# Kernel optimization log

Hardware: AMD Instinct MI355X
Metric: run time of the kernel (lower is better)

## Reference

```python
import jax, jax.numpy as jnp
import numpy as np

H = 128          # hidden / embed dim
NH = 4           # attention heads
HD = H // NH     # head dim = 32
MFD = 4          # missile feat dim
FOD = 15         # full obs dim
NEG_SLOPE = 0.01 # LeakyReLU default


def _gru(x_seq, h0, wih, whh, bih, bhh):
    # x_seq: [B,S,H], h0: [B,H]; torch GRU gate math
    def step(h, x):
        gi = x @ wih.T + bih            # [B,3H]
        gh = h @ whh.T + bhh
        i_r, i_z, i_n = jnp.split(gi, 3, axis=-1)
        h_r, h_z, h_n = jnp.split(gh, 3, axis=-1)
        r = jax.nn.sigmoid(i_r + h_r)
        z = jax.nn.sigmoid(i_z + h_z)
        n = jnp.tanh(i_n + r * h_n)
        h_new = (1.0 - z) * n + z * h
        return h_new, h_new
    h_last, outs = jax.lax.scan(step, h0, jnp.swapaxes(x_seq, 0, 1))
    return jnp.swapaxes(outs, 0, 1), h_last  # [B,S,H], [B,H]


def _ln(x, w, b, eps=1e-5):
    mu = jnp.mean(x, axis=-1, keepdims=True)
    var = jnp.var(x, axis=-1, keepdims=True)
    return (x - mu) * jax.lax.rsqrt(var + eps) * w + b


def setup_inputs() -> dict:
    key = jax.random.key(0)
    ks = jax.random.split(key, 24)
    B, S = 4096, 64
    s = 0.02
    p = {
        "obs": jax.random.normal(ks[0], (B, S, FOD), jnp.float32),
        "h0": jnp.zeros((1, B, H), jnp.float32),
        "enc_air_w": jax.random.normal(ks[1], (H, FOD)) * s,
        "enc_air_b": jnp.zeros((H,)),
        "enc_m_w": jax.random.normal(ks[2], (H, MFD)) * s,
        "enc_m_b": jnp.zeros((H,)),
        "gru_wih": jax.random.normal(ks[3], (3 * H, H)) * s,
        "gru_whh": jax.random.normal(ks[4], (3 * H, H)) * s,
        "gru_bih": jnp.zeros((3 * H,)),
        "gru_bhh": jnp.zeros((3 * H,)),
        "qln_w": jnp.ones((H,)), "qln_b": jnp.zeros((H,)),
        "kln_w": jnp.ones((H,)), "kln_b": jnp.zeros((H,)),
        "attn_in_w": jax.random.normal(ks[5], (3 * H, H)) * s,
        "attn_in_b": jnp.zeros((3 * H,)),
        "attn_out_w": jax.random.normal(ks[6], (H, H)) * s,
        "attn_out_b": jnp.zeros((H,)),
        "mlp0_w": jax.random.normal(ks[7], (H, H)) * s,
        "mlp0_b": jnp.zeros((H,)),
        "mlp1_w": jax.random.normal(ks[8], (H, H)) * s,
        "mlp1_b": jnp.zeros((H,)),
        "fco_w": jax.random.normal(ks[9], (1, H)) * s,
        "fco_b": jnp.zeros((1,)),
    }
    return {k: v.astype(jnp.float32) for k, v in p.items()}


def reference(obs, h0, enc_air_w, enc_air_b, enc_m_w, enc_m_b,
              gru_wih, gru_whh, gru_bih, gru_bhh,
              qln_w, qln_b, kln_w, kln_b,
              attn_in_w, attn_in_b, attn_out_w, attn_out_b,
              mlp0_w, mlp0_b, mlp1_w, mlp1_b, fco_w, fco_b):
    B, S, _ = obs.shape
    N = B * S
    # aircraft encoder + GRU with residual
    air_embed = obs @ enc_air_w.T + enc_air_b                      # [B,S,H]
    gru_out, h_last = _gru(air_embed, h0[0], gru_wih, gru_whh, gru_bih, gru_bhh)
    air_feat = (gru_out + air_embed).reshape(N, H)                 # [N,H]
    # missile encoders (shared weights, two missiles)
    m_raw = obs[..., :2 * MFD].reshape(N, 2, MFD)                  # [N,2,4]
    keys_raw = m_raw @ enc_m_w.T + enc_m_b                         # [N,2,H]
    # inactive-missile mask
    inactive = jnp.array([1.0, 0.0, 1.0, 0.0], obs.dtype)
    mask = jnp.all(jnp.isclose(m_raw, inactive, rtol=1e-5, atol=1e-8), axis=-1)  # [N,2]
    # layer norms
    q_n = _ln(air_feat[:, None, :], qln_w, qln_b)                  # [N,1,H]
    k_n = _ln(keys_raw, kln_w, kln_b)                              # [N,2,H]
    # multihead attention (1 query, 2 keys), values are raw keys
    wq, wk, wv = jnp.split(attn_in_w, 3, axis=0)
    bq, bk, bv = jnp.split(attn_in_b, 3, axis=0)
    q = (q_n @ wq.T + bq).reshape(N, 1, NH, HD)
    k = (k_n @ wk.T + bk).reshape(N, 2, NH, HD)
    v = (keys_raw @ wv.T + bv).reshape(N, 2, NH, HD)
    scores = jnp.einsum('nqhd,nkhd->nhqk', q, k) / jnp.sqrt(jnp.float32(HD))
    scores = scores + jnp.where(mask, -jnp.inf, 0.0)[:, None, None, :]
    attn = jax.nn.softmax(scores, axis=-1)                         # [N,NH,1,2]
    ctx = jnp.einsum('nhqk,nkhd->nqhd', attn, v).reshape(N, H)
    attn_out = ctx @ attn_out_w.T + attn_out_b                     # [N,H]
    attn_out = jnp.where(jnp.isnan(attn_out), 0.0, attn_out)       # nan_to_num guard
    combined = air_feat + attn_out
    # MLP head
    h1 = jax.nn.leaky_relu(combined @ mlp0_w.T + mlp0_b, NEG_SLOPE)
    h2 = jax.nn.leaky_relu(h1 @ mlp1_w.T + mlp1_b, NEG_SLOPE)
    val = h2 @ fco_w.T + fco_b                                     # [N,1]
    return val, h_last[None]
```

## Files before the change

### kernel.cpp

```cpp
#include <hip/hip_runtime.h>
#include <math.h>

#define B_   4096
#define S_   64
#define H_   128
#define N_   (B_*S_)

#define WS_WC    0
#define WS_BC    6144
#define WS_WAP   6528
#define WS_WQP   8576
#define WS_SQ    24960
#define WS_EQ    25088
#define WS_KC    25216
#define WS_EK1   25728
#define WS_SK    25856
#define WS_EK2   25984
#define WS_VC    26112
#define WS_VB    26624
#define WS_MV    26752
#define WS_QQ    26756
#define WS_QLIN  26772
#define WS_MBC   26776
#define WS_C0    26777
#define WS_PB    27392
#define WS_WO2T  (WS_PB + 4096)
#define WS_SROW  (WS_PB + 6784)
#define WS_EROW  (WS_PB + 6812)
#define WS_GB    60160
#define WS_AIR   92928
#define TOKS     32

typedef __attribute__((ext_vector_type(8))) short bf16x8;
typedef __attribute__((ext_vector_type(4))) float f32x4;

__device__ __forceinline__ float dot4(float4 a, float4 b){
    return fmaf(a.x,b.x, fmaf(a.y,b.y, fmaf(a.z,b.z, a.w*b.w)));
}
__device__ __forceinline__ unsigned short f2bf(float f){
    union { float f; unsigned u; } v; v.f = f;
    unsigned r = v.u + 0x7FFF + ((v.u >> 16) & 1);
    return (unsigned short)(r >> 16);
}
__device__ __forceinline__ float bf2f(unsigned short u){
    union { unsigned u; float f; } v; v.u = ((unsigned)u) << 16;
    return v.f;
}

__global__ void precompute_kernel(
    const float* __restrict__ enc_air_w, const float* __restrict__ enc_air_b,
    const float* __restrict__ enc_m_w,  const float* __restrict__ enc_m_b,
    const float* __restrict__ gru_wih,  const float* __restrict__ gru_bih,
    const float* __restrict__ qln_w, const float* __restrict__ qln_b,
    const float* __restrict__ kln_w, const float* __restrict__ kln_b,
    const float* __restrict__ attn_in_w, const float* __restrict__ attn_in_b,
    const float* __restrict__ attn_out_w,
    const float* __restrict__ mlp0_w, const float* __restrict__ mlp1_w,
    float* __restrict__ ws)
{
    int i = blockIdx.x*blockDim.x + threadIdx.x;
    if (i < 6144) {
        int o = i>>4, f = i&15; float a = 0.f;
        if (f < 15) for (int k=0;k<128;k++) a = fmaf(gru_wih[o*128+k], enc_air_w[k*15+f], a);
        ws[WS_WC+i] = a;
    } else if (i < 6528) {
        int o = i-6144; float a = gru_bih[o];
        for (int k=0;k<128;k++) a = fmaf(gru_wih[o*128+k], enc_air_b[k], a);
        ws[WS_BC+o] = a;
    } else if (i < 8576) {
        int idx = i-6528; int j = idx>>4, f = idx&15;
        ws[WS_WAP+idx] = (f<15) ? enc_air_w[j*15+f] : 0.f;
    } else if (i < 24960) {
        int idx = i-8576; int o = idx>>7, j = idx&127;
        ws[WS_WQP+idx] = attn_in_w[o*128+j]*qln_w[j];
    } else if (i < 25088) {
        int o = i-24960; float a=0.f;
        for (int j=0;j<128;j++) a = fmaf(attn_in_w[o*128+j], qln_w[j], a);
        ws[WS_SQ+o]=a;
    } else if (i < 25216) {
        int o = i-25088; float a = attn_in_b[o];
        for (int j=0;j<128;j++) a = fmaf(attn_in_w[o*128+j], qln_b[j], a);
        ws[WS_EQ+o]=a;
    } else if (i < 25728) {
        int idx = i-25216; int o = idx>>2, f = idx&3; float a=0.f;
        for (int j=0;j<128;j++) a = fmaf(attn_in_w[(128+o)*128+j]*kln_w[j], enc_m_w[j*4+f], a);
        ws[WS_KC+idx]=a;
    } else if (i < 25856) {
        int o = i-25728; float a=0.f;
        for (int j=0;j<128;j++) a = fmaf(attn_in_w[(128+o)*128+j]*kln_w[j], enc_m_b[j], a);
        ws[WS_EK1+o]=a;
    } else if (i < 25984) {
        int o = i-25856; float a=0.f;
        for (int j=0;j<128;j++) a = fmaf(attn_in_w[(128+o)*128+j], kln_w[j], a);
        ws[WS_SK+o]=a;
    } else if (i < 26112) {
        int o = i-25984; float a = attn_in_b[128+o];
        for (int j=0;j<128;j++) a = fmaf(attn_in_w[(128+o)*128+j], kln_b[j], a);
        ws[WS_EK2+o]=a;
    } else if (i < 26624) {
        int idx = i-26112; int o = idx>>2, f = idx&3; float a=0.f;
        for (int j=0;j<128;j++) a = fmaf(attn_in_w[(256+o)*128+j], enc_m_w[j*4+f], a);
        ws[WS_VC+idx]=a;
    } else if (i < 26752) {
        int o = i-26624; float a = attn_in_b[256+o];
        for (int j=0;j<128;j++) a = fmaf(attn_in_w[(256+o)*128+j], enc_m_b[j], a);
        ws[WS_VB+o]=a;
    } else if (i < 26756) {
        int f = i-26752; float a=0.f;
        for (int j=0;j<128;j++) a += enc_m_w[j*4+f];
        ws[WS_MV+f]=a*(1.f/128.f);
    } else if (i < 26772) {
        int idx = i-26756; int a4 = idx>>2, b4 = idx&3; float a=0.f;
        for (int j=0;j<128;j++) a = fmaf(enc_m_w[j*4+a4], enc_m_w[j*4+b4], a);
        ws[WS_QQ+idx]=a*(1.f/128.f);
    } else if (i < 26776) {
        int f = i-26772; float a=0.f;
        for (int j=0;j<128;j++) a = fmaf(enc_m_b[j], enc_m_w[j*4+f], a);
        ws[WS_QLIN+f]=a*(2.f/128.f);
    } else if (i == 26776) {
        float a=0.f; for (int j=0;j<128;j++) a += enc_m_b[j];
        ws[WS_MBC]=a*(1.f/128.f);
    } else if (i == 26777) {
        float a=0.f; for (int j=0;j<128;j++) a = fmaf(enc_m_b[j], enc_m_b[j], a);
        ws[WS_C0]=a*(1.f/128.f);
    } else if (i >= 32768 && i < 98304) {
        int idx = i - 32768;
        int mm = idx>>14;
        if (mm >= 2) {
            int i8 = idx & 7, l = (idx>>3)&63, p = (idx>>9)&3, wv = (idx>>11)&7;
            int n = 16*wv + (l&15);
            int k = 32*p + ((l>>4)<<3) + i8;
            float v = (mm==2) ? mlp0_w[n*128+k] : mlp1_w[n*128+k];
            ((unsigned short*)(ws+WS_PB))[idx] = f2bf(v);
        }
    }
}

__global__ void pack_gru_kernel(const float* __restrict__ whh, float* __restrict__ ws)
{
    int idx = blockIdx.x*blockDim.x + threadIdx.x;
    int i8 = idx&7, l=(idx>>3)&63, w=(idx>>9)&7, f=idx>>12;
    int n = 16*w + (l&15);
    int k = ((l>>4)<<3) + i8;
    float v = 0.f;
    if (f < 5) {
        int kk = f*32 + k;
        if (kk < 128) v = whh[n*128 + kk];
        else { int kl = kk-128; if (kl<16) v = ws[WS_WC + n*16 + kl]; }
    } else if (f < 10) {
        int kk = (f-5)*32 + k;
        if (kk < 128) v = whh[(128+n)*128 + kk];
        else { int kl = kk-128; if (kl<16) v = ws[WS_WC + (128+n)*16 + kl]; }
    } else if (f < 14) {
        int kk = (f-10)*32 + k;
        v = whh[(256+n)*128 + kk];
    } else if (f == 14) {
        if (k < 16) v = ws[WS_WC + (256+n)*16 + k];
    } else {
        if (k < 16) v = ws[WS_WAP + n*16 + k];
    }
    ((unsigned short*)(ws+WS_GB))[idx] = f2bf(v);
}

__global__ void pack2_kernel(const float* __restrict__ wo, const float* __restrict__ bo,
                             float* __restrict__ ws)
{
    int i = blockIdx.x*blockDim.x + threadIdx.x;
    if (i < 4096) {
        int i8=i&7, l=(i>>3)&63, p=(i>>9)&3, ct=(i>>11)&1;
        int r = 16*ct + (l&15);
        int k = 32*p + ((l>>4)<<3) + i8;
        float v = 0.f;
        if (r < 28){
            int h = r/7, u = r - h*7;
            float a = 0.f;
            for (int d5=0; d5<32; d5++){
                int d = h*32 + d5;
                float c = (u<4) ? ws[WS_KC + d*4 + u]
                        : (u==4) ? ws[WS_EK1 + d]
                        : (u==5) ? ws[WS_SK + d]
                        :          ws[WS_EK2 + d];
                a = fmaf(c, ws[WS_WQP + d*128 + k], a);
            }
            v = a;
        }
        ((unsigned short*)(ws+WS_PB))[i] = f2bf(v);
    } else if (i < 4152) {
        int j = i - 4096; int r = j % 28; int era = j / 28;
        int h = r/7, u = r - h*7;
        float a = 0.f;
        for (int d5=0; d5<32; d5++){
            int d = h*32 + d5;
            float c = (u<4) ? ws[WS_KC + d*4 + u]
                    : (u==4) ? ws[WS_EK1 + d]
                    : (u==5) ? ws[WS_SK + d]
                    :          ws[WS_EK2 + d];
            a = fmaf(c, ws[(era ? WS_EQ : WS_SQ) + d], a);
        }
        ws[(era ? WS_EROW : WS_SROW) + r] = a;
    } else if (i >= 4224 && i < 6912) {
        int j = i - 4224; int c = j>>7, o = j&127;
        float a;
        if (c == 20) a = bo[o];
        else {
            int h = c/5, u = c - h*5;
            a = 0.f;
            for (int d5=0; d5<32; d5++){
                int d = h*32 + d5;
                float cv = (u<4) ? ws[WS_VC + d*4 + u] : ws[WS_VB + d];
                a = fmaf(wo[o*128 + d], cv, a);
            }
        }
        ws[WS_WO2T + c*128 + o] = a;
    }
}

__global__ void pack3_kernel(const float* __restrict__ mlp0_w, float* __restrict__ ws)
{
    int i = blockIdx.x*blockDim.x + threadIdx.x;
    int i8=i&7, l=(i>>3)&63, w=(i>>9)&7;
    int n = 16*w + (l&15);
    int c = ((l>>4)<<3) + i8;
    float v = 0.f;
    if (c < 21){
        float a = 0.f;
        const float* wo2 = ws + WS_WO2T + c*128;
        for (int o=0;o<128;o++) a = fmaf(mlp0_w[n*128+o], wo2[o], a);
        v = a;
    }
    ((unsigned short*)(ws+WS_PB))[4096 + i] = f2bf(v);
}

__global__ __launch_bounds__(512) void gru_kernel(
    const float* __restrict__ obs, const float* __restrict__ h0,
    const float* __restrict__ bhh, const float* __restrict__ ba,
    const float* __restrict__ ws,
    unsigned short* __restrict__ air, float* __restrict__ out)
{
    __shared__ __align__(16) unsigned short Abf[2][16*136];
    __shared__ __align__(16) unsigned short obs_lds[64*16*24];
    __shared__ __align__(16) unsigned short zero16[8];

    const int t = threadIdx.x;
    const int w = t>>6;
    const int l = t&63;
    const int quad = l>>4;
    const int col  = l&15;
    const int jj   = 16*w + col;
    const int row0 = blockIdx.x*16;

    const unsigned short* gb = (const unsigned short*)(ws + WS_GB);
    bf16x8 bf[16];
    #pragma unroll
    for (int f=0; f<16; f++) bf[f] = *(const bf16x8*)&gb[(f*8 + w)*512 + l*8];

    const float bcrt = ws[WS_BC+jj]     + bhh[jj];
    const float bczt = ws[WS_BC+128+jj] + bhh[128+jj];
    const float bcn  = ws[WS_BC+256+jj];
    const float bhn  = bhh[256+jj];
    const float baj  = ba[jj];

    float hreg[4];
    #pragma unroll
    for (int reg=0; reg<4; reg++)
        hreg[reg] = h0[(size_t)(row0+quad*4+reg)*128 + jj];

    if (t < 8) zero16[t] = 0;

    {
        int rr = t>>5, c0 = (t&31)*4;
        float4 hv = *(const float4*)&h0[(size_t)(row0+rr)*128 + c0];
        unsigned long long pk = (unsigned long long)f2bf(hv.x)
              | ((unsigned long long)f2bf(hv.y)<<16)
              | ((unsigned long long)f2bf(hv.z)<<32)
              | ((unsigned long long)f2bf(hv.w)<<48);
        *(unsigned long long*)&Abf[0][rr*136 + c0] = pk;
    }

    #pragma unroll
    for (int it=0; it<8; it++){
        int pair = it*128 + (t>>2);
        int sub  = t&3;
        int tok = pair>>6, s = pair&63;
        const float* op = &obs[((size_t)(row0+tok)*64 + s)*15 + sub*4];
        unsigned long long pk = 0;
        #pragma unroll
        for (int k=0;k<4;k++){
            int c = sub*4+k;
            float ov = (c<15) ? op[k] : 0.f;
            pk |= ((unsigned long long)f2bf(ov)) << (16*k);
        }
        *(unsigned long long*)&obs_lds[(s*16+tok)*24 + sub*4] = pk;
    }
    __syncthreads();

    for (int s=0; s<64; s++){
        const unsigned short* Ac = Abf[s&1];
        unsigned short*       An = Abf[(s+1)&1];

        bf16x8 a0 = *(const bf16x8*)&Ac[col*136 +  0 + quad*8];
        bf16x8 a1 = *(const bf16x8*)&Ac[col*136 + 32 + quad*8];
        bf16x8 a2 = *(const bf16x8*)&Ac[col*136 + 64 + quad*8];
        bf16x8 a3 = *(const bf16x8*)&Ac[col*136 + 96 + quad*8];
        const unsigned short* osrc = (quad<2)
            ? &obs_lds[(s*16+col)*24 + quad*8] : &zero16[0];
        bf16x8 a4 = *(const bf16x8*)osrc;

        f32x4 aR = {0.f,0.f,0.f,0.f};
        f32x4 aZ = {0.f,0.f,0.f,0.f};
        f32x4 aN = {0.f,0.f,0.f,0.f};
        f32x4 aG = {0.f,0.f,0.f,0.f};
        f32x4 aE = {0.f,0.f,0.f,0.f};
        aR = __builtin_amdgcn_mfma_f32_16x16x32_bf16(a0, bf[0],  aR, 0,0,0);
        aR = __builtin_amdgcn_mfma_f32_16x16x32_bf16(a1, bf[1],  aR, 0,0,0);
        aR = __builtin_amdgcn_mfma_f32_16x16x32_bf16(a2, bf[2],  aR, 0,0,0);
        aR = __builtin_amdgcn_mfma_f32_16x16x32_bf16(a3, bf[3],  aR, 0,0,0);
        aR = __builtin_amdgcn_mfma_f32_16x16x32_bf16(a4, bf[4],  aR, 0,0,0);
        aZ = __builtin_amdgcn_mfma_f32_16x16x32_bf16(a0, bf[5],  aZ, 0,0,0);
        aZ = __builtin_amdgcn_mfma_f32_16x16x32_bf16(a1, bf[6],  aZ, 0,0,0);
        aZ = __builtin_amdgcn_mfma_f32_16x16x32_bf16(a2, bf[7],  aZ, 0,0,0);
        aZ = __builtin_amdgcn_mfma_f32_16x16x32_bf16(a3, bf[8],  aZ, 0,0,0);
        aZ = __builtin_amdgcn_mfma_f32_16x16x32_bf16(a4, bf[9],  aZ, 0,0,0);
        aN = __builtin_amdgcn_mfma_f32_16x16x32_bf16(a0, bf[10], aN, 0,0,0);
        aN = __builtin_amdgcn_mfma_f32_16x16x32_bf16(a1, bf[11], aN, 0,0,0);
        aN = __builtin_amdgcn_mfma_f32_16x16x32_bf16(a2, bf[12], aN, 0,0,0);
        aN = __builtin_amdgcn_mfma_f32_16x16x32_bf16(a3, bf[13], aN, 0,0,0);
        aG = __builtin_amdgcn_mfma_f32_16x16x32_bf16(a4, bf[14], aG, 0,0,0);
        aE = __builtin_amdgcn_mfma_f32_16x16x32_bf16(a4, bf[15], aE, 0,0,0);

        #pragma unroll
        for (int reg=0; reg<4; reg++){
            int tok = quad*4 + reg;
            float rg = __builtin_amdgcn_rcpf(1.f + __expf(-(aR[reg] + bcrt)));
            float zg = __builtin_amdgcn_rcpf(1.f + __expf(-(aZ[reg] + bczt)));
            float nx = fmaf(rg, aN[reg] + bhn, aG[reg] + bcn);
            float e2 = __expf(2.f*nx);
            float ng = 1.f - 2.f*__builtin_amdgcn_rcpf(e2 + 1.f);
            float hn = fmaf(zg, hreg[reg]-ng, ng);
            hreg[reg] = hn;
            An[tok*136 + jj] = f2bf(hn);
            air[((size_t)(row0+tok)*64 + s)*128 + jj] = f2bf(hn + (aE[reg] + baj));
        }
        if (s==63){
            #pragma unroll
            for (int reg=0; reg<4; reg++)
                out[(size_t)N_ + (size_t)(row0+quad*4+reg)*128 + jj] = hreg[reg];
        }
        asm volatile("s_waitcnt lgkmcnt(0)" ::: "memory");
        __builtin_amdgcn_s_barrier();
        __builtin_amdgcn_sched_barrier(0);
    }
}

__global__ __launch_bounds__(512) void attnmlp_kernel(
    const float* __restrict__ obs,
    const float* __restrict__ ws,
    const float* __restrict__ b0, const float* __restrict__ b1,
    const float* __restrict__ fcw, const float* __restrict__ fcb,
    const unsigned short* __restrict__ air, float* __restrict__ out)
{
    __shared__ __align__(16) unsigned short U_bf[TOKS*168];
    __shared__ __align__(16) unsigned short H1_bf[TOKS*136];
    __shared__ float praw[TOKS*28];
    __shared__ float obs_m[TOKS][8];
    __shared__ float mu_s[TOKS], rs_s[TOKS];
    __shared__ float kmu_s[TOKS][2], krs_s[TOKS][2];
    __shared__ int   kmask_s[TOKS][2];

    const int t = threadIdx.x;
    const int w = t>>6;
    const int l = t&63;
    const int quad = l>>4;
    const int col  = l&15;
    const int jj   = 16*w + col;
    const int n0 = blockIdx.x*TOKS;

    const unsigned short* pb = (const unsigned short*)(ws + WS_PB);

    {
        const int tok0 = t>>4, sub = t&15;
        const unsigned short* ap = &air[(size_t)(n0+tok0)*128 + sub*8];
        uint4 xv = *(const uint4*)ap;
        *(uint4*)&U_bf[tok0*168 + sub*8] = xv;
        float sm = 0.f, s2 = 0.f;
        #pragma unroll
        for (int q4=0;q4<4;q4++){
            unsigned qv = ((const unsigned*)&xv)[q4];
            float a = bf2f((unsigned short)(qv & 0xFFFF));
            float b = bf2f((unsigned short)(qv >> 16));
            sm += a + b;
            s2 = fmaf(a,a, fmaf(b,b, s2));
        }
        #pragma unroll
        for (int m=1;m<16;m<<=1){ sm += __shfl_xor(sm,m); s2 += __shfl_xor(s2,m); }
        if (sub==0){
            float mu = sm*(1.f/128.f);
            float var = s2*(1.f/128.f) - mu*mu;
            mu_s[tok0]=mu; rs_s[tok0]=rsqrtf(var+1e-5f);
        }
        if (sub<5){
            #pragma unroll
            for (int c=0;c<4;c++) U_bf[tok0*168 + 148 + sub*4 + c] = 0;
        }
        if (sub<8) obs_m[tok0][sub] = obs[(size_t)(n0+tok0)*15 + sub];
    }
    if (t < 64){
        int rr = t>>1, mi = t&1;
        const float* mp = &obs[(size_t)(n0+rr)*15 + mi*4];
        float m0=mp[0], m1=mp[1], m2=mp[2], m3=mp[3];
        const float tol1 = 1e-8f + 1e-5f, tol0 = 1e-8f;
        kmask_s[rr][mi] = (fabsf(m0-1.f)<=tol1)&&(fabsf(m1)<=tol0)&&
                          (fabsf(m2-1.f)<=tol1)&&(fabsf(m3)<=tol0);
        float mv[4]={m0,m1,m2,m3};
        float mu = ws[WS_MBC];
        #pragma unroll
        for (int f=0;f<4;f++) mu = fmaf(ws[WS_MV+f], mv[f], mu);
        float e2 = ws[WS_C0];
        #pragma unroll
        for (int a4=0;a4<4;a4++){
            e2 = fmaf(ws[WS_QLIN+a4], mv[a4], e2);
            #pragma unroll
            for (int b4=0;b4<4;b4++) e2 = fmaf(ws[WS_QQ+a4*4+b4]*mv[a4], mv[b4], e2);
        }
        float var = e2 - mu*mu;
        kmu_s[rr][mi]=mu; krs_s[rr][mi]=rsqrtf(var+1e-5f);
    }
    __syncthreads();

    if (w < 4){
        const int tt = w>>1, ct = w&1;
        const int jA = ct*16 + col;
        f32x4 acc = {0.f,0.f,0.f,0.f};
        #pragma unroll
        for (int p=0;p<4;p++){
            bf16x8 a = *(const bf16x8*)&U_bf[(tt*16+col)*168 + p*32 + quad*8];
            bf16x8 b = *(const bf16x8*)&pb[((ct*4+p)*64 + l)*8];
            acc = __builtin_amdgcn_mfma_f32_16x16x32_bf16(a, b, acc, 0,0,0);
        }
        if (jA < 28){
            const float Sr = ws[WS_SROW + jA], Er = ws[WS_EROW + jA];
            #pragma unroll
            for (int reg=0;reg<4;reg++){
                int tok = tt*16 + quad*4 + reg;
                praw[tok*28 + jA] = fmaf(rs_s[tok], acc[reg] - mu_s[tok]*Sr, Er);
            }
        }
    }
    __syncthreads();

    if (t < TOKS*4){
        const int tok = t>>2, h = t&3;
        const float* pr = &praw[tok*28 + h*7];
        const float T0=pr[0],T1=pr[1],T2=pr[2],T3=pr[3],Pa=pr[4],Pb=pr[5],Pc=pr[6];
        const float4 m0v = *(const float4*)&obs_m[tok][0];
        const float4 m1v = *(const float4*)&obs_m[tok][4];
        const float scale = 0.17677669529663687f;
        float d0 = fmaf(T0,m0v.x, fmaf(T1,m0v.y, fmaf(T2,m0v.z, fmaf(T3,m0v.w, Pa))));
        float d1 = fmaf(T0,m1v.x, fmaf(T1,m1v.y, fmaf(T2,m1v.z, fmaf(T3,m1v.w, Pa))));
        float s0 = fmaf(krs_s[tok][0], d0 - kmu_s[tok][0]*Pb, Pc) * scale;
        float s1 = fmaf(krs_s[tok][1], d1 - kmu_s[tok][1]*Pb, Pc) * scale;
        int msk0 = kmask_s[tok][0], msk1 = kmask_s[tok][1];
        float a0, a1;
        if (msk0 && msk1){
            a0=0.f; a1=0.f;
            if (h==0) U_bf[tok*168 + 148] = 0;
        } else {
            if (h==0) U_bf[tok*168 + 148] = 0x3F80;
            if (msk0)      { a0=0.f; a1=1.f; }
            else if (msk1) { a0=1.f; a1=0.f; }
            else {
                float mx = fmaxf(s0,s1);
                float e0 = __expf(s0-mx), e1 = __expf(s1-mx);
                float inv = 1.f/(e0+e1);
                a0 = e0*inv; a1 = e1*inv;
            }
        }
        int cb = tok*168 + 128 + h*5;
        U_bf[cb+0] = f2bf(fmaf(a0, m0v.x, a1*m1v.x));
        U_bf[cb+1] = f2bf(fmaf(a0, m0v.y, a1*m1v.y));
        U_bf[cb+2] = f2bf(fmaf(a0, m0v.z, a1*m1v.z));
        U_bf[cb+3] = f2bf(fmaf(a0, m0v.w, a1*m1v.w));
        U_bf[cb+4] = f2bf(a0 + a1);
    }
    __syncthreads();

    {
        bf16x8 bfr[5];
        #pragma unroll
        for (int p=0;p<4;p++) bfr[p] = *(const bf16x8*)&pb[((2*32 + w*4 + p)*64 + l)*8];
        bfr[4] = *(const bf16x8*)&pb[4096 + (w*64 + l)*8];
        f32x4 acc[2];
        #pragma unroll
        for (int tt=0;tt<2;tt++) acc[tt] = (f32x4){0.f,0.f,0.f,0.f};
        #pragma unroll
        for (int p=0;p<5;p++){
            const int ko = p*32 + quad*8;
            #pragma unroll
            for (int tt=0;tt<2;tt++){
                bf16x8 a = *(const bf16x8*)&U_bf[(tt*16+col)*168 + ko];
                acc[tt] = __builtin_amdgcn_mfma_f32_16x16x32_bf16(a, bfr[p], acc[tt], 0,0,0);
            }
        }
        const float b0j = b0[jj];
        #pragma unroll
        for (int tt=0;tt<2;tt++){
            #pragma unroll
            for (int reg=0;reg<4;reg++){
                int tok = tt*16 + quad*4 + reg;
                float v = acc[tt][reg] + b0j;
                v = (v > 0.f) ? v : 0.01f*v;
                H1_bf[tok*136 + jj] = f2bf(v);
            }
        }
    }
    __syncthreads();

    {
        bf16x8 bfr[4];
        #pragma unroll
        for (int p=0;p<4;p++) bfr[p] = *(const bf16x8*)&pb[((3*32 + w*4 + p)*64 + l)*8];
        f32x4 acc[2];
        #pragma unroll
        for (int tt=0;tt<2;tt++) acc[tt] = (f32x4){0.f,0.f,0.f,0.f};
        #pragma unroll
        for (int p=0;p<4;p++){
            const int ko = p*32 + quad*8;
            #pragma unroll
            for (int tt=0;tt<2;tt++){
                bf16x8 a = *(const bf16x8*)&H1_bf[(tt*16+col)*136 + ko];
                acc[tt] = __builtin_amdgcn_mfma_f32_16x16x32_bf16(a, bfr[p], acc[tt], 0,0,0);
            }
        }
        const float b1j = b1[jj], fcj = fcw[jj];
        float pv[8];
        #pragma unroll
        for (int tt=0;tt<2;tt++){
            #pragma unroll
            for (int reg=0;reg<4;reg++){
                float v = acc[tt][reg] + b1j;
                v = (v > 0.f) ? v : 0.01f*v;
                pv[tt*4+reg] = v * fcj;
            }
        }
        #pragma unroll
        for (int m=1;m<16;m<<=1){
            #pragma unroll
            for (int q2=0;q2<8;q2++) pv[q2] += __shfl_xor(pv[q2], m);
        }
        if (col==0){
            #pragma unroll
            for (int tt=0;tt<2;tt++){
                #pragma unroll
                for (int reg=0;reg<4;reg++)
                    praw[(tt*16 + quad*4 + reg)*8 + w] = pv[tt*4+reg];
            }
        }
    }
    __syncthreads();

    if (t < TOKS){
        float a = fcb[0];
        #pragma unroll
        for (int k=0;k<8;k++) a += praw[t*8 + k];
        out[n0 + t] = a;
    }
}

extern "C" void kernel_launch(void* const* d_in, const int* in_sizes, int n_in,
                              void* d_out, int out_size, void* d_ws, size_t ws_size,
                              hipStream_t stream) {
    const float* obs       = (const float*)d_in[0];
    const float* h0        = (const float*)d_in[1];
    const float* enc_air_w = (const float*)d_in[2];
    const float* enc_air_b = (const float*)d_in[3];
    const float* enc_m_w   = (const float*)d_in[4];
    const float* enc_m_b   = (const float*)d_in[5];
    const float* gru_wih   = (const float*)d_in[6];
    const float* gru_whh   = (const float*)d_in[7];
    const float* gru_bih   = (const float*)d_in[8];
    const float* gru_bhh   = (const float*)d_in[9];
    const float* qln_w     = (const float*)d_in[10];
    const float* qln_b     = (const float*)d_in[11];
    const float* kln_w     = (const float*)d_in[12];
    const float* kln_b     = (const float*)d_in[13];
    const float* attn_in_w = (const float*)d_in[14];
    const float* attn_in_b = (const float*)d_in[15];
    const float* attn_out_w= (const float*)d_in[16];
    const float* attn_out_b= (const float*)d_in[17];
    const float* mlp0_w    = (const float*)d_in[18];
    const float* mlp0_b    = (const float*)d_in[19];
    const float* mlp1_w    = (const float*)d_in[20];
    const float* mlp1_b    = (const float*)d_in[21];
    const float* fco_w     = (const float*)d_in[22];
    const float* fco_b     = (const float*)d_in[23];
    float* out = (float*)d_out;
    float* ws  = (float*)d_ws;
    unsigned short* air = (unsigned short*)(ws + WS_AIR);

    precompute_kernel<<<dim3(384), dim3(256), 0, stream>>>(
        enc_air_w, enc_air_b, enc_m_w, enc_m_b, gru_wih, gru_bih,
        qln_w, qln_b, kln_w, kln_b, attn_in_w, attn_in_b,
        attn_out_w, mlp0_w, mlp1_w, ws);

    pack_gru_kernel<<<dim3(256), dim3(256), 0, stream>>>(gru_whh, ws);
    pack2_kernel<<<dim3(27), dim3(256), 0, stream>>>(attn_out_w, attn_out_b, ws);
    pack3_kernel<<<dim3(16), dim3(256), 0, stream>>>(mlp0_w, ws);

    gru_kernel<<<dim3(256), dim3(512), 0, stream>>>(
        obs, h0, gru_bhh, enc_air_b, ws, air, out);

    attnmlp_kernel<<<dim3(N_/TOKS), dim3(512), 0, stream>>>(
        obs, ws, mlp0_b, mlp1_b, fco_w, fco_b, air, out);
}
```

Measured before the change: 251.4 us.

## Pipeline GRU input MFMAs, double attn-MLP tile, move LN stats and final projection to MFMA

The GRU loop now computes the obs-projection MFMAs for step s+1 during step s, so they leave the recurrent critical path. It also strength-reduces the air store address and writes the final hidden state once after the loop. The attention/MLP kernel processes 64 tokens per block instead of 32. Layer-norm sum and sum-of-squares are computed with MFMAs (a ones column in the packed weights plus a self-product), replacing shuffle reductions. The final fc dot product becomes an MFMA against a packed fco_w matrix instead of a cross-lane shuffle reduction. These cut per-step latency and reduction overhead, at the cost of more registers and LDS per block and a changed workspace layout.

```diff
diff --git a/kernel.cpp b/kernel.cpp
--- a/kernel.cpp
+++ b/kernel.cpp
@@ -24,12 +24,12 @@
 #define WS_MBC   26776
 #define WS_C0    26777
 #define WS_PB    27392
-#define WS_WO2T  (WS_PB + 4096)
-#define WS_SROW  (WS_PB + 6784)
-#define WS_EROW  (WS_PB + 6812)
+#define WS_WO2T  (WS_PB + 5120)
+#define WS_SROW  (WS_PB + 7808)
+#define WS_EROW  (WS_PB + 7836)
 #define WS_GB    60160
 #define WS_AIR   92928
-#define TOKS     32
+#define TOKS     64
 
 typedef __attribute__((ext_vector_type(8))) short bf16x8;
 typedef __attribute__((ext_vector_type(4))) float f32x4;
@@ -183,6 +183,8 @@
                 a = fmaf(c, ws[WS_WQP + d*128 + k], a);
             }
             v = a;
+        } else if (r == 31) {
+            v = 1.f;
         }
         ((unsigned short*)(ws+WS_PB))[i] = f2bf(v);
     } else if (i < 4152) {
@@ -215,20 +217,30 @@
     }
 }
 
-__global__ void pack3_kernel(const float* __restrict__ mlp0_w, float* __restrict__ ws)
+__global__ void pack3_kernel(const float* __restrict__ mlp0_w,
+                             const float* __restrict__ fcw,
+                             float* __restrict__ ws)
 {
     int i = blockIdx.x*blockDim.x + threadIdx.x;
-    int i8=i&7, l=(i>>3)&63, w=(i>>9)&7;
-    int n = 16*w + (l&15);
-    int c = ((l>>4)<<3) + i8;
-    float v = 0.f;
-    if (c < 21){
-        float a = 0.f;
-        const float* wo2 = ws + WS_WO2T + c*128;
-        for (int o=0;o<128;o++) a = fmaf(mlp0_w[n*128+o], wo2[o], a);
-        v = a;
-    }
-    ((unsigned short*)(ws+WS_PB))[4096 + i] = f2bf(v);
+    if (i < 4096){
+        int i8=i&7, l=(i>>3)&63, w=(i>>9)&7;
+        int n = 16*w + (l&15);
+        int c = ((l>>4)<<3) + i8;
+        float v = 0.f;
+        if (c < 21){
+            float a = 0.f;
+            const float* wo2 = ws + WS_WO2T + c*128;
+            for (int o=0;o<128;o++) a = fmaf(mlp0_w[n*128+o], wo2[o], a);
+            v = a;
+        }
+        ((unsigned short*)(ws+WS_PB))[4096 + i] = f2bf(v);
+    } else {
+        int j = i - 4096;
+        int i8=j&7, l=(j>>3)&63, p=(j>>9)&3;
+        int k = 32*p + ((l>>4)<<3) + i8;
+        float v = ((l&15)==0) ? fcw[k] : 0.f;
+        ((unsigned short*)(ws+WS_PB))[8192 + j] = f2bf(v);
+    }
 }
 
 __global__ __launch_bounds__(512) void gru_kernel(
@@ -294,6 +306,20 @@
     }
     __syncthreads();
 
+    unsigned short* ap = air + (size_t)(row0 + quad*4)*8192 + jj;
+
+    f32x4 oR, oZ, oG, oE;
+    {
+        const unsigned short* osrc = (quad<2)
+            ? &obs_lds[(0*16+col)*24 + quad*8] : &zero16[0];
+        bf16x8 a4 = *(const bf16x8*)osrc;
+        f32x4 z = {0.f,0.f,0.f,0.f};
+        oR = __builtin_amdgcn_mfma_f32_16x16x32_bf16(a4, bf[4],  z, 0,0,0);
+        oZ = __builtin_amdgcn_mfma_f32_16x16x32_bf16(a4, bf[9],  z, 0,0,0);
+        oG = __builtin_amdgcn_mfma_f32_16x16x32_bf16(a4, bf[14], z, 0,0,0);
+        oE = __builtin_amdgcn_mfma_f32_16x16x32_bf16(a4, bf[15], z, 0,0,0);
+    }
+
     for (int s=0; s<64; s++){
         const unsigned short* Ac = Abf[s&1];
         unsigned short*       An = Abf[(s+1)&1];
@@ -302,70 +328,75 @@
         bf16x8 a1 = *(const bf16x8*)&Ac[col*136 + 32 + quad*8];
         bf16x8 a2 = *(const bf16x8*)&Ac[col*136 + 64 + quad*8];
         bf16x8 a3 = *(const bf16x8*)&Ac[col*136 + 96 + quad*8];
-        const unsigned short* osrc = (quad<2)
-            ? &obs_lds[(s*16+col)*24 + quad*8] : &zero16[0];
-        bf16x8 a4 = *(const bf16x8*)osrc;
-
-        f32x4 aR = {0.f,0.f,0.f,0.f};
-        f32x4 aZ = {0.f,0.f,0.f,0.f};
+
+        f32x4 aR = oR, aZ = oZ;
         f32x4 aN = {0.f,0.f,0.f,0.f};
-        f32x4 aG = {0.f,0.f,0.f,0.f};
-        f32x4 aE = {0.f,0.f,0.f,0.f};
         aR = __builtin_amdgcn_mfma_f32_16x16x32_bf16(a0, bf[0],  aR, 0,0,0);
         aR = __builtin_amdgcn_mfma_f32_16x16x32_bf16(a1, bf[1],  aR, 0,0,0);
         aR = __builtin_amdgcn_mfma_f32_16x16x32_bf16(a2, bf[2],  aR, 0,0,0);
         aR = __builtin_amdgcn_mfma_f32_16x16x32_bf16(a3, bf[3],  aR, 0,0,0);
-        aR = __builtin_amdgcn_mfma_f32_16x16x32_bf16(a4, bf[4],  aR, 0,0,0);
         aZ = __builtin_amdgcn_mfma_f32_16x16x32_bf16(a0, bf[5],  aZ, 0,0,0);
         aZ = __builtin_amdgcn_mfma_f32_16x16x32_bf16(a1, bf[6],  aZ, 0,0,0);
         aZ = __builtin_amdgcn_mfma_f32_16x16x32_bf16(a2, bf[7],  aZ, 0,0,0);
         aZ = __builtin_amdgcn_mfma_f32_16x16x32_bf16(a3, bf[8],  aZ, 0,0,0);
-        aZ = __builtin_amdgcn_mfma_f32_16x16x32_bf16(a4, bf[9],  aZ, 0,0,0);
         aN = __builtin_amdgcn_mfma_f32_16x16x32_bf16(a0, bf[10], aN, 0,0,0);
         aN = __builtin_amdgcn_mfma_f32_16x16x32_bf16(a1, bf[11], aN, 0,0,0);
         aN = __builtin_amdgcn_mfma_f32_16x16x32_bf16(a2, bf[12], aN, 0,0,0);
         aN = __builtin_amdgcn_mfma_f32_16x16x32_bf16(a3, bf[13], aN, 0,0,0);
-        aG = __builtin_amdgcn_mfma_f32_16x16x32_bf16(a4, bf[14], aG, 0,0,0);
-        aE = __builtin_amdgcn_mfma_f32_16x16x32_bf16(a4, bf[15], aE, 0,0,0);
+
+        f32x4 nR, nZ, nG, nE;
+        if (s < 63){
+            const unsigned short* osrc = (quad<2)
+                ? &obs_lds[((s+1)*16+col)*24 + quad*8] : &zero16[0];
+            bf16x8 a4 = *(const bf16x8*)osrc;
+            f32x4 z = {0.f,0.f,0.f,0.f};
+            nR = __builtin_amdgcn_mfma_f32_16x16x32_bf16(a4, bf[4],  z, 0,0,0);
+            nZ = __builtin_amdgcn_mfma_f32_16x16x32_bf16(a4, bf[9],  z, 0,0,0);
+            nG = __builtin_amdgcn_mfma_f32_16x16x32_bf16(a4, bf[14], z, 0,0,0);
+            nE = __builtin_amdgcn_mfma_f32_16x16x32_bf16(a4, bf[15], z, 0,0,0);
+        }
 
         #pragma unroll
         for (int reg=0; reg<4; reg++){
             int tok = quad*4 + reg;
             float rg = __builtin_amdgcn_rcpf(1.f + __expf(-(aR[reg] + bcrt)));
             float zg = __builtin_amdgcn_rcpf(1.f + __expf(-(aZ[reg] + bczt)));
-            float nx = fmaf(rg, aN[reg] + bhn, aG[reg] + bcn);
+            float nx = fmaf(rg, aN[reg] + bhn, oG[reg] + bcn);
             float e2 = __expf(2.f*nx);
             float ng = 1.f - 2.f*__builtin_amdgcn_rcpf(e2 + 1.f);
             float hn = fmaf(zg, hreg[reg]-ng, ng);
             hreg[reg] = hn;
             An[tok*136 + jj] = f2bf(hn);
-            air[((size_t)(row0+tok)*64 + s)*128 + jj] = f2bf(hn + (aE[reg] + baj));
-        }
-        if (s==63){
-            #pragma unroll
-            for (int reg=0; reg<4; reg++)
-                out[(size_t)N_ + (size_t)(row0+quad*4+reg)*128 + jj] = hreg[reg];
-        }
+            ap[(size_t)reg*8192] = f2bf(hn + (oE[reg] + baj));
+        }
+        ap += 128;
+        if (s < 63){ oR = nR; oZ = nZ; oG = nG; oE = nE; }
+
         asm volatile("s_waitcnt lgkmcnt(0)" ::: "memory");
         __builtin_amdgcn_s_barrier();
         __builtin_amdgcn_sched_barrier(0);
     }
+
+    #pragma unroll
+    for (int reg=0; reg<4; reg++)
+        out[(size_t)N_ + (size_t)(row0+quad*4+reg)*128 + jj] = hreg[reg];
 }
 
 __global__ __launch_bounds__(512) void attnmlp_kernel(
     const float* __restrict__ obs,
     const float* __restrict__ ws,
     const float* __restrict__ b0, const float* __restrict__ b1,
-    const float* __restrict__ fcw, const float* __restrict__ fcb,
+    const float* __restrict__ fcb,
     const unsigned short* __restrict__ air, float* __restrict__ out)
 {
     __shared__ __align__(16) unsigned short U_bf[TOKS*168];
     __shared__ __align__(16) unsigned short H1_bf[TOKS*136];
     __shared__ float praw[TOKS*28];
     __shared__ float obs_m[TOKS][8];
-    __shared__ float mu_s[TOKS], rs_s[TOKS];
+    __shared__ float sm_s[TOKS], s2_s[TOKS];
     __shared__ float kmu_s[TOKS][2], krs_s[TOKS][2];
     __shared__ int   kmask_s[TOKS][2];
+    __shared__ float sero[56];
 
     const int t = threadIdx.x;
     const int w = t>>6;
@@ -378,33 +409,19 @@
     const unsigned short* pb = (const unsigned short*)(ws + WS_PB);
 
     {
-        const int tok0 = t>>4, sub = t&15;
-        const unsigned short* ap = &air[(size_t)(n0+tok0)*128 + sub*8];
-        uint4 xv = *(const uint4*)ap;
-        *(uint4*)&U_bf[tok0*168 + sub*8] = xv;
-        float sm = 0.f, s2 = 0.f;
-        #pragma unroll
-        for (int q4=0;q4<4;q4++){
-            unsigned qv = ((const unsigned*)&xv)[q4];
-            float a = bf2f((unsigned short)(qv & 0xFFFF));
-            float b = bf2f((unsigned short)(qv >> 16));
-            sm += a + b;
-            s2 = fmaf(a,a, fmaf(b,b, s2));
-        }
-        #pragma unroll
-        for (int m=1;m<16;m<<=1){ sm += __shfl_xor(sm,m); s2 += __shfl_xor(s2,m); }
-        if (sub==0){
-            float mu = sm*(1.f/128.f);
-            float var = s2*(1.f/128.f) - mu*mu;
-            mu_s[tok0]=mu; rs_s[tok0]=rsqrtf(var+1e-5f);
-        }
-        if (sub<5){
+        const int tok0 = t>>3, sub = t&7;
+        const unsigned short* apx = &air[(size_t)(n0+tok0)*128 + sub*16];
+        uint4 x0 = *(const uint4*)apx;
+        uint4 x1 = *(const uint4*)(apx+8);
+        *(uint4*)&U_bf[tok0*168 + sub*16]     = x0;
+        *(uint4*)&U_bf[tok0*168 + sub*16 + 8] = x1;
+        if (sub < 5){
             #pragma unroll
             for (int c=0;c<4;c++) U_bf[tok0*168 + 148 + sub*4 + c] = 0;
         }
-        if (sub<8) obs_m[tok0][sub] = obs[(size_t)(n0+tok0)*15 + sub];
-    }
-    if (t < 64){
+        obs_m[tok0][sub] = obs[(size_t)(n0+tok0)*15 + sub];
+    }
+    if (t < 128){
         int rr = t>>1, mi = t&1;
         const float* mp = &obs[(size_t)(n0+rr)*15 + mi*4];
         float m0=mp[0], m1=mp[1], m2=mp[2], m3=mp[3];
@@ -425,33 +442,50 @@
         float var = e2 - mu*mu;
         kmu_s[rr][mi]=mu; krs_s[rr][mi]=rsqrtf(var+1e-5f);
     }
+    if (t < 56) sero[t] = ws[WS_SROW + t];
     __syncthreads();
 
-    if (w < 4){
+    {
         const int tt = w>>1, ct = w&1;
         const int jA = ct*16 + col;
+        bf16x8 afr[4];
+        #pragma unroll
+        for (int p=0;p<4;p++)
+            afr[p] = *(const bf16x8*)&U_bf[(tt*16+col)*168 + p*32 + quad*8];
         f32x4 acc = {0.f,0.f,0.f,0.f};
         #pragma unroll
-        for (int p=0;p<4;p++){
-            bf16x8 a = *(const bf16x8*)&U_bf[(tt*16+col)*168 + p*32 + quad*8];
-            bf16x8 b = *(const bf16x8*)&pb[((ct*4+p)*64 + l)*8];
-            acc = __builtin_amdgcn_mfma_f32_16x16x32_bf16(a, b, acc, 0,0,0);
+        for (int p=0;p<4;p++)
+            acc = __builtin_amdgcn_mfma_f32_16x16x32_bf16(afr[p], *(const bf16x8*)&pb[((ct*4+p)*64 + l)*8], acc, 0,0,0);
+        if (ct == 1){
+            f32x4 accX = {0.f,0.f,0.f,0.f};
+            #pragma unroll
+            for (int p=0;p<4;p++)
+                accX = __builtin_amdgcn_mfma_f32_16x16x32_bf16(afr[p], afr[p], accX, 0,0,0);
+            if ((col>>2) == quad) s2_s[tt*16+col] = accX[col&3];
+            if (col == 15){
+                #pragma unroll
+                for (int reg=0;reg<4;reg++) sm_s[tt*16+quad*4+reg] = acc[reg];
+            }
         }
         if (jA < 28){
-            const float Sr = ws[WS_SROW + jA], Er = ws[WS_EROW + jA];
-            #pragma unroll
-            for (int reg=0;reg<4;reg++){
-                int tok = tt*16 + quad*4 + reg;
-                praw[tok*28 + jA] = fmaf(rs_s[tok], acc[reg] - mu_s[tok]*Sr, Er);
-            }
+            #pragma unroll
+            for (int reg=0;reg<4;reg++)
+                praw[(tt*16+quad*4+reg)*28 + jA] = acc[reg];
         }
     }
     __syncthreads();
 
     if (t < TOKS*4){
         const int tok = t>>2, h = t&3;
+        float mu = sm_s[tok]*(1.f/128.f);
+        float var = s2_s[tok]*(1.f/128.f) - mu*mu;
+        float rs = rsqrtf(var + 1e-5f);
         const float* pr = &praw[tok*28 + h*7];
-        const float T0=pr[0],T1=pr[1],T2=pr[2],T3=pr[3],Pa=pr[4],Pb=pr[5],Pc=pr[6];
+        float P[7];
+        #pragma unroll
+        for (int u=0;u<7;u++)
+            P[u] = fmaf(rs, pr[u] - mu*sero[h*7+u], sero[28 + h*7+u]);
+        const float T0=P[0],T1=P[1],T2=P[2],T3=P[3],Pa=P[4],Pb=P[5],Pc=P[6];
         const float4 m0v = *(const float4*)&obs_m[tok][0];
         const float4 m1v = *(const float4*)&obs_m[tok][4];
         const float scale = 0.17677669529663687f;
@@ -489,21 +523,21 @@
         #pragma unroll
         for (int p=0;p<4;p++) bfr[p] = *(const bf16x8*)&pb[((2*32 + w*4 + p)*64 + l)*8];
         bfr[4] = *(const bf16x8*)&pb[4096 + (w*64 + l)*8];
-        f32x4 acc[2];
-        #pragma unroll
-        for (int tt=0;tt<2;tt++) acc[tt] = (f32x4){0.f,0.f,0.f,0.f};
+        f32x4 acc[4];
+        #pragma unroll
+        for (int tt=0;tt<4;tt++) acc[tt] = (f32x4){0.f,0.f,0.f,0.f};
         #pragma unroll
         for (int p=0;p<5;p++){
             const int ko = p*32 + quad*8;
             #pragma unroll
-            for (int tt=0;tt<2;tt++){
+            for (int tt=0;tt<4;tt++){
                 bf16x8 a = *(const bf16x8*)&U_bf[(tt*16+col)*168 + ko];
                 acc[tt] = __builtin_amdgcn_mfma_f32_16x16x32_bf16(a, bfr[p], acc[tt], 0,0,0);
             }
         }
         const float b0j = b0[jj];
         #pragma unroll
-        for (int tt=0;tt<2;tt++){
+        for (int tt=0;tt<4;tt++){
             #pragma unroll
             for (int reg=0;reg<4;reg++){
                 int tok = tt*16 + quad*4 + reg;
@@ -519,50 +553,46 @@
         bf16x8 bfr[4];
         #pragma unroll
         for (int p=0;p<4;p++) bfr[p] = *(const bf16x8*)&pb[((3*32 + w*4 + p)*64 + l)*8];
-        f32x4 acc[2];
-        #pragma unroll
-        for (int tt=0;tt<2;tt++) acc[tt] = (f32x4){0.f,0.f,0.f,0.f};
+        f32x4 acc[4];
+        #pragma unroll
+        for (int tt=0;tt<4;tt++) acc[tt] = (f32x4){0.f,0.f,0.f,0.f};
         #pragma unroll
         for (int p=0;p<4;p++){
             const int ko = p*32 + quad*8;
             #pragma unroll
-            for (int tt=0;tt<2;tt++){
+            for (int tt=0;tt<4;tt++){
                 bf16x8 a = *(const bf16x8*)&H1_bf[(tt*16+col)*136 + ko];
                 acc[tt] = __builtin_amdgcn_mfma_f32_16x16x32_bf16(a, bfr[p], acc[tt], 0,0,0);
             }
         }
-        const float b1j = b1[jj], fcj = fcw[jj];
-        float pv[8];
-        #pragma unroll
-        for (int tt=0;tt<2;tt++){
+        const float b1j = b1[jj];
+        #pragma unroll
+        for (int tt=0;tt<4;tt++){
             #pragma unroll
             for (int reg=0;reg<4;reg++){
+                int tok = tt*16 + quad*4 + reg;
                 float v = acc[tt][reg] + b1j;
                 v = (v > 0.f) ? v : 0.01f*v;
-                pv[tt*4+reg] = v * fcj;
-            }
-        }
-        #pragma unroll
-        for (int m=1;m<16;m<<=1){
-            #pragma unroll
-            for (int q2=0;q2<8;q2++) pv[q2] += __shfl_xor(pv[q2], m);
-        }
-        if (col==0){
-            #pragma unroll
-            for (int tt=0;tt<2;tt++){
-                #pragma unroll
-                for (int reg=0;reg<4;reg++)
-                    praw[(tt*16 + quad*4 + reg)*8 + w] = pv[tt*4+reg];
+                U_bf[tok*168 + jj] = f2bf(v);
             }
         }
     }
     __syncthreads();
 
-    if (t < TOKS){
-        float a = fcb[0];
-        #pragma unroll
-        for (int k=0;k<8;k++) a += praw[t*8 + k];
-        out[n0 + t] = a;
+    if (w < 4){
+        f32x4 acc = {0.f,0.f,0.f,0.f};
+        #pragma unroll
+        for (int p=0;p<4;p++){
+            bf16x8 a = *(const bf16x8*)&U_bf[(w*16+col)*168 + p*32 + quad*8];
+            bf16x8 b = *(const bf16x8*)&pb[8192 + (p*64 + l)*8];
+            acc = __builtin_amdgcn_mfma_f32_16x16x32_bf16(a, b, acc, 0,0,0);
+        }
+        if (col == 0){
+            float fb = fcb[0];
+            #pragma unroll
+            for (int reg=0;reg<4;reg++)
+                out[n0 + w*16 + quad*4 + reg] = acc[reg] + fb;
+        }
     }
 }
 
@@ -604,11 +634,11 @@
 
     pack_gru_kernel<<<dim3(256), dim3(256), 0, stream>>>(gru_whh, ws);
     pack2_kernel<<<dim3(27), dim3(256), 0, stream>>>(attn_out_w, attn_out_b, ws);
-    pack3_kernel<<<dim3(16), dim3(256), 0, stream>>>(mlp0_w, ws);
+    pack3_kernel<<<dim3(24), dim3(256), 0, stream>>>(mlp0_w, fco_w, ws);
 
     gru_kernel<<<dim3(256), dim3(512), 0, stream>>>(
         obs, h0, gru_bhh, enc_air_b, ws, air, out);
 
     attnmlp_kernel<<<dim3(N_/TOKS), dim3(512), 0, stream>>>(
-        obs, ws, mlp0_b, mlp1_b, fco_w, fco_b, air, out);
-}
+        obs, ws, mlp0_b, mlp1_b, fco_b, air, out);
+}
```

After: 230.8 us. 1.09x faster.
